# Performance work log

Hardware: AMD Instinct MI355X
Metric: run time of the kernel (lower is better)

## Reference

```python
import jax, jax.numpy as jnp
import numpy as np

B, SQ, SKV, D, H = 4, 2048, 2048, 1024, 16
DH = D // H  # 64


def setup_inputs() -> dict:
    key = jax.random.key(0)
    ks = jax.random.split(key, 8)
    s = 0.02  # realistic init scale for weights
    return {
        "query": jax.random.normal(ks[0], (B, SQ, D), dtype=jnp.float32),
        "value": jax.random.normal(ks[1], (B, SKV, D), dtype=jnp.float32),
        "wq": jax.random.normal(ks[2], (H, D, DH), dtype=jnp.float32) * s,
        "bq": jnp.zeros((H, DH), dtype=jnp.float32),
        "wk": jax.random.normal(ks[3], (H, D, DH), dtype=jnp.float32) * s,
        "bk": jnp.zeros((H, DH), dtype=jnp.float32),
        "wv": jax.random.normal(ks[4], (H, D, DH), dtype=jnp.float32) * s,
        "bv": jnp.zeros((H, DH), dtype=jnp.float32),
        "wo": jax.random.normal(ks[5], (D, D), dtype=jnp.float32) * s,
        "bo": jnp.zeros((D,), dtype=jnp.float32),
    }


def reference(query, value, wq, bq, wk, bk, wv, bv, wo, bo):
    # Batched equivalent of the per-head Dense loop: [B,S,D] x [H,D,DH] -> [B,H,S,DH]
    q = jnp.einsum("bsd,hde->bhse", query, wq) + bq[None, :, None, :]
    k = jnp.einsum("bsd,hde->bhse", value, wk) + bk[None, :, None, :]
    v = jnp.einsum("bsd,hde->bhse", value, wv) + bv[None, :, None, :]
    scale = 1.0 / jnp.sqrt(jnp.asarray(DH, dtype=q.dtype))
    scores = jnp.einsum("bhqe,bhke->bhqk", q, k) * scale  # [B,H,SQ,SKV]
    align = jax.nn.softmax(scores, axis=-1)
    heads = jnp.einsum("bhqk,bhke->bhqe", align, v)  # [B,H,SQ,DH]
    # concat heads along feature dim (head order preserved)
    heads = jnp.transpose(heads, (0, 2, 1, 3)).reshape(B, SQ, D)
    return heads @ wo + bo
```

## Files before the change

kernel.cpp:

```cpp
#include <hip/hip_runtime.h>
#include <stdint.h>

#define DEVI __device__ __forceinline__

typedef __bf16  bf16x8 __attribute__((ext_vector_type(8)));
typedef float   f32x4  __attribute__((ext_vector_type(4)));
typedef float   f32x16 __attribute__((ext_vector_type(16)));
typedef uint32_t u32x4 __attribute__((ext_vector_type(4)));
typedef uint32_t u32x2v __attribute__((ext_vector_type(2)));
typedef uint16_t u16x8 __attribute__((ext_vector_type(8)));
typedef uint16_t u16x4 __attribute__((ext_vector_type(4)));

static constexpr int BB = 4, SQL = 2048, SKVL = 2048, DMODEL = 1024, NH = 16;
static constexpr int MROWS = BB * SQL;
static constexpr int KD = DMODEL;

DEVI uint16_t f2bf(float x) {
  uint32_t u = __builtin_bit_cast(uint32_t, x);
  u += 0x7FFFu + ((u >> 16) & 1u);
  return (uint16_t)(u >> 16);
}
DEVI uint32_t cvt2bf(float a, float b) {
  __bf16 x = (__bf16)a, y = (__bf16)b;
  return (uint32_t)__builtin_bit_cast(uint16_t, x) |
         ((uint32_t)__builtin_bit_cast(uint16_t, y) << 16);
}
DEVI f32x4 mfma16(bf16x8 a, bf16x8 b, f32x4 c) {
  return __builtin_amdgcn_mfma_f32_16x16x32_bf16(a, b, c, 0, 0, 0);
}
DEVI f32x16 mfma32(bf16x8 a, bf16x8 b, f32x16 c) {
  return __builtin_amdgcn_mfma_f32_32x32x16_bf16(a, b, c, 0, 0, 0);
}
DEVI void gload16(const void* g, void* l) {
  __builtin_amdgcn_global_load_lds((__attribute__((address_space(1))) const void*)g,
                                   (__attribute__((address_space(3))) void*)l, 16, 0, 0);
}
DEVI bf16x8 ldread(const void* p) { return __builtin_bit_cast(bf16x8, *(const u32x4*)p); }
DEVI u32x2v plswap(uint32_t a, uint32_t b) {
  return __builtin_amdgcn_permlane32_swap(a, b, false, false);
}

__global__ __launch_bounds__(256) void k_cvt(const float* __restrict__ q, const float* __restrict__ v,
                                             const float* __restrict__ wq, const float* __restrict__ wk,
                                             const float* __restrict__ wv, const float* __restrict__ wo,
                                             uint16_t* __restrict__ aq, uint16_t* __restrict__ av,
                                             uint16_t* __restrict__ wt) {
  const int bx = blockIdx.x;
  const int tid = threadIdx.x;
  if (bx < 1024) {
    __shared__ float lds[64 * 65];
    const float* src; int rstride; size_t obase; int d0;
    if (bx < 768) {
      const int zz = bx >> 8, rem = bx & 255, h = rem >> 4, dt = rem & 15;
      d0 = dt * 64;
      src = ((zz == 0) ? wq : (zz == 1) ? wk : wv) + (size_t)h * 65536;
      rstride = 64;
      obase = (size_t)zz * 1048576 + (size_t)h * 64 * 1024;
    } else {
      const int idx = bx - 768, dt = idx >> 4, nt = idx & 15;
      d0 = dt * 64;
      src = wo + nt * 64;
      rstride = 1024;
      obase = (size_t)3 * 1048576 + (size_t)(nt * 64) * 1024;
    }
    const int e4 = (tid & 15) * 4, dl0 = tid >> 4;
    #pragma unroll
    for (int p = 0; p < 4; ++p) {
      const int dl = dl0 + p * 16;
      const float4 x = *(const float4*)(src + (size_t)(d0 + dl) * rstride + e4);
      float* row = &lds[dl * 65 + e4];
      row[0] = x.x; row[1] = x.y; row[2] = x.z; row[3] = x.w;
    }
    __syncthreads();
    const int er = tid >> 2, dp = tid & 3;
    uint16_t tmp[16];
    #pragma unroll
    for (int i = 0; i < 16; ++i) tmp[i] = f2bf(lds[(dp * 16 + i) * 65 + er]);
    uint16_t* orow = wt + obase + (size_t)er * 1024 + d0 + dp * 16;
    u16x8 o0, o1;
    #pragma unroll
    for (int j = 0; j < 8; ++j) { o0[j] = tmp[j]; o1[j] = tmp[8 + j]; }
    *(u16x8*)orow = o0;
    *(u16x8*)(orow + 8) = o1;
  } else {
    const int64_t n4 = (int64_t)MROWS * DMODEL / 4;
    for (int64_t i = (int64_t)(bx - 1024) * 256 + tid; i < 2 * n4; i += (int64_t)2048 * 256) {
      const bool second = (i >= n4);
      const int64_t j = second ? i - n4 : i;
      const float4 x = (second ? (const float4*)v : (const float4*)q)[j];
      u16x4 o = { f2bf(x.x), f2bf(x.y), f2bf(x.z), f2bf(x.w) };
      *(u16x4*)((second ? av : aq) + j * 4) = o;
    }
  }
}

__global__ __launch_bounds__(256) void k_gemm3(const uint16_t* __restrict__ Aq, const uint16_t* __restrict__ Av,
                                               const uint16_t* __restrict__ Wt,
                                               const float* __restrict__ bq, const float* __restrict__ bk,
                                               const float* __restrict__ bv,
                                               uint16_t* __restrict__ Qb, uint16_t* __restrict__ Kb,
                                               uint16_t* __restrict__ Vt, float qscale) {
  __shared__ __align__(16) uint16_t SM[4][128 * 64];
  const int tid = threadIdx.x;
  const int w = tid >> 6, ln = tid & 63;
  const int g = ln >> 4, lc = ln & 15;
  const int bid = blockIdx.x;
  const int xm = bid & 7, rr = bid >> 3;
  const int yy = rr % 24, xh = rr / 24;
  const int x = xh * 8 + xm;
  const int seg = yy >> 3;
  const int m0 = x * 128, n0 = (yy & 7) * 128;
  const uint16_t* A = (seg == 0) ? Aq : Av;
  const uint16_t* Bt = Wt + (size_t)seg * 1048576;
  const float* bias = (seg == 0) ? bq : (seg == 1) ? bk : bv;
  const float oscale = (seg == 0) ? qscale : 1.0f;
  const int wm = (w >> 1) * 64, wn = (w & 1) * 64;
  const int srow = w * 32 + (ln >> 3);
  const int colp = (ln & 7) * 16;

  f32x4 acc[4][4] = {};

  auto stage = [&](int kt, int bs) {
    #pragma unroll
    for (int i = 0; i < 4; ++i) {
      const int row = srow + i * 8;
      const int colb = colp ^ ((row & 7) << 4);
      gload16((const char*)(A + (size_t)(m0 + row) * KD + kt * 64) + colb,
              (char*)&SM[bs][0] + w * 4096 + i * 1024);
      gload16((const char*)(Bt + (size_t)(n0 + row) * KD + kt * 64) + colb,
              (char*)&SM[2 + bs][0] + w * 4096 + i * 1024);
    }
  };

  stage(0, 0);
  asm volatile("s_waitcnt vmcnt(0)" ::: "memory");
  __builtin_amdgcn_s_barrier();
  __builtin_amdgcn_sched_barrier(0);

  int cur = 0;
  #pragma unroll 2
  for (int kt = 0; kt < KD / 64; ++kt) {
    if (kt + 1 < KD / 64) stage(kt + 1, cur ^ 1);
    const char* Ac = (const char*)&SM[cur][0];
    const char* Bc = (const char*)&SM[2 + cur][0];
    #pragma unroll
    for (int kk = 0; kk < 2; ++kk) {
      bf16x8 af[4], bfr[4];
      #pragma unroll
      for (int mt = 0; mt < 4; ++mt) {
        const int row = wm + mt * 16 + lc;
        af[mt] = ldread(Ac + row * 128 + ((kk * 64 + g * 16) ^ ((row & 7) << 4)));
      }
      #pragma unroll
      for (int nt = 0; nt < 4; ++nt) {
        const int row = wn + nt * 16 + lc;
        bfr[nt] = ldread(Bc + row * 128 + ((kk * 64 + g * 16) ^ ((row & 7) << 4)));
      }
      #pragma unroll
      for (int mt = 0; mt < 4; ++mt)
        #pragma unroll
        for (int nt = 0; nt < 4; ++nt)
          acc[mt][nt] = mfma16(af[mt], bfr[nt], acc[mt][nt]);
    }
    asm volatile("s_waitcnt vmcnt(0)" ::: "memory");
    __builtin_amdgcn_s_barrier();
    __builtin_amdgcn_sched_barrier(0);
    cur ^= 1;
  }

  uint16_t* ldc = &SM[0][0];
  const int bb = m0 >> 11;
  const int s_base = m0 & 2047;
  const int h0 = n0 >> 6;
  if (seg != 2) {
    #pragma unroll
    for (int nt = 0; nt < 4; ++nt) {
      const int n = n0 + wn + nt * 16 + lc;
      const float bv_ = bias[n];
      #pragma unroll
      for (int mt = 0; mt < 4; ++mt) {
        #pragma unroll
        for (int r = 0; r < 4; ++r) {
          const int row = wm + mt * 16 + g * 4 + r;
          ldc[row * 136 + wn + nt * 16 + lc] = f2bf((acc[mt][nt][r] + bv_) * oscale);
        }
      }
    }
    __syncthreads();
    uint16_t* outp = (seg == 0) ? Qb : Kb;
    #pragma unroll
    for (int j = 0; j < 8; ++j) {
      const int idx = j * 256 + tid;
      const int row = idx >> 4, slot = idx & 15;
      const int h = h0 + (slot >> 3);
      const int e = (slot & 7) * 8;
      const u16x8 val = *(const u16x8*)(ldc + row * 136 + slot * 8);
      *(u16x8*)(outp + (((size_t)(bb * NH + h) * SQL) + s_base + row) * 64 + e) = val;
    }
  } else {
    #pragma unroll
    for (int nt = 0; nt < 4; ++nt) {
      const int n = n0 + wn + nt * 16 + lc;
      const float bv_ = bias[n];
      #pragma unroll
      for (int mt = 0; mt < 4; ++mt) {
        #pragma unroll
        for (int r = 0; r < 4; ++r) {
          const int row = wm + mt * 16 + g * 4 + r;
          ldc[(wn + nt * 16 + lc) * 136 + row] = f2bf(acc[mt][nt][r] + bv_);
        }
      }
    }
    __syncthreads();
    #pragma unroll
    for (int j = 0; j < 8; ++j) {
      const int idx = j * 256 + tid;
      const int er = idx >> 4, slot = idx & 15;
      const int h = h0 + (er >> 6);
      const int e = er & 63;
      const u16x8 val = *(const u16x8*)(ldc + er * 136 + slot * 8);
      *(u16x8*)(Vt + ((size_t)(bb * NH + h) * 64 + e) * SKVL + s_base + slot * 8) = val;
    }
  }
}

__global__ __launch_bounds__(256) void k_gemmO(const uint16_t* __restrict__ A, const uint16_t* __restrict__ Bt,
                                               const float* __restrict__ bias, float* __restrict__ outp) {
  __shared__ __align__(16) uint16_t Al[2][128 * 64];
  __shared__ __align__(16) uint16_t Bl[2][128 * 64];
  const int tid = threadIdx.x;
  const int w = tid >> 6, ln = tid & 63;
  const int g = ln >> 4, lc = ln & 15;
  const int bid = blockIdx.x;
  const int xm = bid & 7, rr = bid >> 3;
  const int yy = rr & 7, xh = rr >> 3;
  const int m0 = (xh * 8 + xm) * 128, n0 = yy * 128;
  const int wm = (w >> 1) * 64, wn = (w & 1) * 64;
  const int srow = w * 32 + (ln >> 3);
  const int colp = (ln & 7) * 16;

  f32x4 acc[4][4] = {};

  auto stage = [&](int kt, int bs) {
    #pragma unroll
    for (int i = 0; i < 4; ++i) {
      const int row = srow + i * 8;
      const int colb = colp ^ ((row & 7) << 4);
      gload16((const char*)(A + (size_t)(m0 + row) * KD + kt * 64) + colb,
              (char*)&Al[bs][0] + w * 4096 + i * 1024);
      gload16((const char*)(Bt + (size_t)(n0 + row) * KD + kt * 64) + colb,
              (char*)&Bl[bs][0] + w * 4096 + i * 1024);
    }
  };

  stage(0, 0);
  asm volatile("s_waitcnt vmcnt(0)" ::: "memory");
  __builtin_amdgcn_s_barrier();
  __builtin_amdgcn_sched_barrier(0);

  int cur = 0;
  #pragma unroll 2
  for (int kt = 0; kt < KD / 64; ++kt) {
    if (kt + 1 < KD / 64) stage(kt + 1, cur ^ 1);
    const char* Ac = (const char*)&Al[cur][0];
    const char* Bc = (const char*)&Bl[cur][0];
    #pragma unroll
    for (int kk = 0; kk < 2; ++kk) {
      bf16x8 af[4], bfr[4];
      #pragma unroll
      for (int mt = 0; mt < 4; ++mt) {
        const int row = wm + mt * 16 + lc;
        af[mt] = ldread(Ac + row * 128 + ((kk * 64 + g * 16) ^ ((row & 7) << 4)));
      }
      #pragma unroll
      for (int nt = 0; nt < 4; ++nt) {
        const int row = wn + nt * 16 + lc;
        bfr[nt] = ldread(Bc + row * 128 + ((kk * 64 + g * 16) ^ ((row & 7) << 4)));
      }
      #pragma unroll
      for (int mt = 0; mt < 4; ++mt)
        #pragma unroll
        for (int nt = 0; nt < 4; ++nt)
          acc[mt][nt] = mfma16(af[mt], bfr[nt], acc[mt][nt]);
    }
    asm volatile("s_waitcnt vmcnt(0)" ::: "memory");
    __builtin_amdgcn_s_barrier();
    __builtin_amdgcn_sched_barrier(0);
    cur ^= 1;
  }

  #pragma unroll
  for (int nt = 0; nt < 4; ++nt) {
    const int n = n0 + wn + nt * 16 + lc;
    const float bv_ = bias[n];
    #pragma unroll
    for (int mt = 0; mt < 4; ++mt) {
      #pragma unroll
      for (int r = 0; r < 4; ++r) {
        const int m = m0 + wm + mt * 16 + g * 4 + r;
        outp[(size_t)m * DMODEL + n] = acc[mt][nt][r] + bv_;
      }
    }
  }
}

__global__ __launch_bounds__(256, 3) void k_attn(const uint16_t* __restrict__ Qb,
                                                 const uint16_t* __restrict__ Kb,
                                                 const uint16_t* __restrict__ Vt,
                                                 uint16_t* __restrict__ Hd) {
  __shared__ __align__(16) uint16_t Kl[2][64 * 64];
  __shared__ __align__(16) uint16_t Vl[2][64 * 64];
  const int tid = threadIdx.x;
  const int w = tid >> 6, ln = tid & 63;
  const int ql = ln & 31, hi = ln >> 5;
  const int bsw = blockIdx.x;
  const int l = (bsw & 7) * 128 + (bsw >> 3);
  const int qx = l & 15, bh = l >> 4;
  const int q0 = qx * 128 + w * 32;

  const uint16_t* Qp = Qb + ((size_t)bh * SQL + q0 + ql) * 64;
  bf16x8 qf[4];
  #pragma unroll
  for (int s = 0; s < 4; ++s)
    qf[s] = __builtin_bit_cast(bf16x8, *(const u16x8*)(Qp + s * 16 + hi * 8));

  const uint16_t* Kbase = Kb + (size_t)bh * SKVL * 64;
  const uint16_t* Vtb = Vt + (size_t)bh * 64 * SKVL;

  const int swl = (ln & 7) << 4;
  const int e0off = (hi << 4) ^ swl;
  const int rb = ql * 128;

  const int krow0 = w * 16 + (ln >> 3);
  const int kcolb = (((ln & 7) ^ (ln >> 3)) << 4);
  const int vslot = ((ln & 7) ^ (ln >> 3)) * 8;

  f32x16 acc0 = {}, acc1 = {};
  float lsum = 0.f;

  auto stageK = [&](int t, int buf) {
    const uint16_t* Kc = Kbase + (size_t)t * 4096;
    #pragma unroll
    for (int i = 0; i < 2; ++i)
      gload16((const char*)(Kc + (size_t)(krow0 + i * 8) * 64) + kcolb,
              (char*)&Kl[buf][0] + w * 2048 + i * 1024);
  };
  auto stageV = [&](int t, int buf) {
    const uint16_t* Vc = Vtb + (size_t)t * 64 + vslot;
    #pragma unroll
    for (int i = 0; i < 2; ++i)
      gload16((const char*)(Vc + (size_t)(krow0 + i * 8) * SKVL),
              (char*)&Vl[buf][0] + w * 2048 + i * 1024);
  };

  stageK(0, 0);
  stageV(0, 0);
  __syncthreads();

  int cur = 0;
  for (int t = 0; t < SKVL / 64; ++t) {
    const bool pre = (t + 1 < SKVL / 64);
    if (pre) {
      stageK(t + 1, cur ^ 1);
      stageV(t + 1, cur ^ 1);
    }
    const char* Kc0 = (const char*)&Kl[cur][0];
    f32x16 s0 = {}, s1 = {};
    __builtin_amdgcn_s_setprio(1);
    #pragma unroll
    for (int s = 0; s < 4; ++s) {
      const int off = e0off ^ (s << 5);
      const bf16x8 k0 = ldread(Kc0 + rb + off);
      const bf16x8 k1 = ldread(Kc0 + 4096 + rb + off);
      s0 = mfma32(k0, qf[s], s0);
      s1 = mfma32(k1, qf[s], s1);
    }
    __builtin_amdgcn_s_setprio(0);
    float ps = 0.f;
    #pragma unroll
    for (int r = 0; r < 16; ++r) {
      s0[r] = __builtin_amdgcn_exp2f(s0[r]);
      s1[r] = __builtin_amdgcn_exp2f(s1[r]);
      ps += s0[r] + s1[r];
    }
    lsum += ps;
    uint32_t w32[2][4][2];
    #pragma unroll
    for (int c8 = 0; c8 < 4; ++c8) {
      #pragma unroll
      for (int p = 0; p < 2; ++p) {
        w32[0][c8][p] = cvt2bf(s0[4 * c8 + 2 * p], s0[4 * c8 + 2 * p + 1]);
        w32[1][c8][p] = cvt2bf(s1[4 * c8 + 2 * p], s1[4 * c8 + 2 * p + 1]);
      }
    }
    const char* Vc0 = (const char*)&Vl[cur][0];
    __builtin_amdgcn_s_setprio(1);
    #pragma unroll
    for (int u = 0; u < 4; ++u) {
      const int tt = u >> 1, ul = u & 1;
      const u32x2v e0 = plswap(w32[tt][2 * ul][0], w32[tt][2 * ul + 1][0]);
      const u32x2v e1 = plswap(w32[tt][2 * ul][1], w32[tt][2 * ul + 1][1]);
      u32x4 pj;
      pj[0] = e0[0]; pj[1] = e1[0]; pj[2] = e0[1]; pj[3] = e1[1];
      const bf16x8 pb = __builtin_bit_cast(bf16x8, pj);
      const int off = e0off ^ (u << 5);
      const bf16x8 v0 = ldread(Vc0 + rb + off);
      const bf16x8 v1 = ldread(Vc0 + 4096 + rb + off);
      acc0 = mfma32(v0, pb, acc0);
      acc1 = mfma32(v1, pb, acc1);
    }
    __builtin_amdgcn_s_setprio(0);
    __syncthreads();
    cur ^= 1;
  }
  {
    const float lt = lsum + __shfl_xor(lsum, 32);
    const float inv = __builtin_amdgcn_rcpf(lt);
    const int b = bh >> 4, h = bh & 15;
    uint16_t* op = Hd + ((size_t)(b * SQL + q0 + ql)) * DMODEL + h * 64;
    #pragma unroll
    for (int et = 0; et < 2; ++et) {
      #pragma unroll
      for (int r2 = 0; r2 < 8; ++r2) {
        const float v0 = (et ? acc1[2 * r2] : acc0[2 * r2]) * inv;
        const float v1 = (et ? acc1[2 * r2 + 1] : acc0[2 * r2 + 1]) * inv;
        const int e = et * 32 + 4 * hi + (r2 & 1) * 2 + (r2 >> 1) * 8;
        *(uint32_t*)(op + e) = cvt2bf(v0, v1);
      }
    }
  }
}

extern "C" void kernel_launch(void* const* d_in, const int* in_sizes, int n_in,
                              void* d_out, int out_size, void* d_ws, size_t ws_size,
                              hipStream_t stream) {
  const float* query = (const float*)d_in[0];
  const float* value = (const float*)d_in[1];
  const float* wq = (const float*)d_in[2];
  const float* bq = (const float*)d_in[3];
  const float* wk = (const float*)d_in[4];
  const float* bk = (const float*)d_in[5];
  const float* wv = (const float*)d_in[6];
  const float* bv = (const float*)d_in[7];
  const float* wo = (const float*)d_in[8];
  const float* bo = (const float*)d_in[9];

  const size_t SZ_ACT = (size_t)MROWS * DMODEL * 2;
  const size_t SZ_W   = (size_t)4 * DMODEL * DMODEL * 2;
  if (ws_size < 6 * SZ_ACT + SZ_W) return;

  char* ws = (char*)d_ws;
  uint16_t* Aq = (uint16_t*)ws;  ws += SZ_ACT;
  uint16_t* Av = (uint16_t*)ws;  ws += SZ_ACT;
  uint16_t* Wt = (uint16_t*)ws;  ws += SZ_W;
  uint16_t* Qb = (uint16_t*)ws;  ws += SZ_ACT;
  uint16_t* Kb = (uint16_t*)ws;  ws += SZ_ACT;
  uint16_t* Vtw = (uint16_t*)ws; ws += SZ_ACT;
  uint16_t* Hd = (uint16_t*)ws;  ws += SZ_ACT;

  const float QSCALE = 0.18033688011112042f;

  k_cvt<<<dim3(3072), dim3(256), 0, stream>>>(query, value, wq, wk, wv, wo, Aq, Av, Wt);
  k_gemm3<<<dim3(1536), dim3(256), 0, stream>>>(Aq, Av, Wt, bq, bk, bv, Qb, Kb, Vtw, QSCALE);
  k_attn<<<dim3(1024), dim3(256), 0, stream>>>(Qb, Kb, Vtw, Hd);
  k_gemmO<<<dim3(512), dim3(256), 0, stream>>>(Hd, Wt + 3145728, bo, (float*)d_out);
}
```

Before: 198.4 us.

## Deepen attention K/V staging to four LDS buffers with vmcnt-based waits

The attention kernel moves from a double-buffered K/V LDS pipeline to a four-deep ring. Loads for chunk t+3 are issued while chunk t is computed. The full `__syncthreads` is replaced by explicit `s_waitcnt vmcnt` counts plus a raw barrier, so only the oldest outstanding chunk is waited on, and the loop is unrolled with a hand-written drain tail. This is meant to hide more global-load latency behind the MFMA work. In exchange, LDS per block doubles to 64KB, which may lower the number of resident blocks per CU below the launch-bounds target of 3.

After: 208.9 us. 1.05x slower.

```diff
diff --git a/kernel.cpp b/kernel.cpp
--- a/kernel.cpp
+++ b/kernel.cpp
@@ -308,8 +308,8 @@
                                                  const uint16_t* __restrict__ Kb,
                                                  const uint16_t* __restrict__ Vt,
                                                  uint16_t* __restrict__ Hd) {
-  __shared__ __align__(16) uint16_t Kl[2][64 * 64];
-  __shared__ __align__(16) uint16_t Vl[2][64 * 64];
+  __shared__ __align__(16) uint16_t Kl[4][64 * 64];
+  __shared__ __align__(16) uint16_t Vl[4][64 * 64];
   const int tid = threadIdx.x;
   const int w = tid >> 6, ln = tid & 63;
   const int ql = ln & 31, hi = ln >> 5;
@@ -352,19 +352,8 @@
       gload16((const char*)(Vc + (size_t)(krow0 + i * 8) * SKVL),
               (char*)&Vl[buf][0] + w * 2048 + i * 1024);
   };
-
-  stageK(0, 0);
-  stageV(0, 0);
-  __syncthreads();
-
-  int cur = 0;
-  for (int t = 0; t < SKVL / 64; ++t) {
-    const bool pre = (t + 1 < SKVL / 64);
-    if (pre) {
-      stageK(t + 1, cur ^ 1);
-      stageV(t + 1, cur ^ 1);
-    }
-    const char* Kc0 = (const char*)&Kl[cur][0];
+  auto computeChunk = [&](int buf) {
+    const char* Kc0 = (const char*)&Kl[buf][0];
     f32x16 s0 = {}, s1 = {};
     __builtin_amdgcn_s_setprio(1);
     #pragma unroll
@@ -393,7 +382,7 @@
         w32[1][c8][p] = cvt2bf(s1[4 * c8 + 2 * p], s1[4 * c8 + 2 * p + 1]);
       }
     }
-    const char* Vc0 = (const char*)&Vl[cur][0];
+    const char* Vc0 = (const char*)&Vl[buf][0];
     __builtin_amdgcn_s_setprio(1);
     #pragma unroll
     for (int u = 0; u < 4; ++u) {
@@ -410,9 +399,39 @@
       acc1 = mfma32(v1, pb, acc1);
     }
     __builtin_amdgcn_s_setprio(0);
-    __syncthreads();
-    cur ^= 1;
-  }
+  };
+
+  stageK(0, 0); stageV(0, 0);
+  stageK(1, 1); stageV(1, 1);
+  stageK(2, 2); stageV(2, 2);
+  asm volatile("s_waitcnt vmcnt(8)" ::: "memory");
+  __builtin_amdgcn_s_barrier();
+  __builtin_amdgcn_sched_barrier(0);
+
+  #pragma unroll 4
+  for (int t = 0; t < 28; ++t) {
+    stageK(t + 3, (t + 3) & 3);
+    stageV(t + 3, (t + 3) & 3);
+    computeChunk(t & 3);
+    asm volatile("s_waitcnt vmcnt(8)" ::: "memory");
+    __builtin_amdgcn_s_barrier();
+    __builtin_amdgcn_sched_barrier(0);
+  }
+  stageK(31, 3); stageV(31, 3);
+  computeChunk(0);
+  asm volatile("s_waitcnt vmcnt(8)" ::: "memory");
+  __builtin_amdgcn_s_barrier();
+  __builtin_amdgcn_sched_barrier(0);
+  computeChunk(1);
+  asm volatile("s_waitcnt vmcnt(4)" ::: "memory");
+  __builtin_amdgcn_s_barrier();
+  __builtin_amdgcn_sched_barrier(0);
+  computeChunk(2);
+  asm volatile("s_waitcnt vmcnt(0)" ::: "memory");
+  __builtin_amdgcn_s_barrier();
+  __builtin_amdgcn_sched_barrier(0);
+  computeChunk(3);
+
   {
     const float lt = lsum + __shfl_xor(lsum, 32);
     const float inv = __builtin_amdgcn_rcpf(lt);
```
